# Performance work log

Hardware: AMD Instinct MI355X
Metric: run time of the kernel (lower is better)

The kernel has to match this reference:

```python
import jax, jax.numpy as jnp
import numpy as np

NUM_HEADS = 1


def setup_inputs() -> dict:
    key = jax.random.key(0)
    k1, k2, k3 = jax.random.split(key, 3)
    B, C, H, W = 32, 1024, 32, 32
    x = jax.random.normal(k1, (B, C, H, W), dtype=jnp.float32)
    w_qkv = jax.random.normal(k2, (3 * C, C), dtype=jnp.float32) * (C ** -0.5)
    w_proj = jax.random.normal(k3, (C, C), dtype=jnp.float32) * (C ** -0.5)
    b_proj = jnp.zeros((C,), dtype=jnp.float32)
    return {"x": x, "w_qkv": w_qkv, "w_proj": w_proj, "b_proj": b_proj}


def reference(x, w_qkv, w_proj, b_proj):
    B, C, H, W = x.shape
    nh = NUM_HEADS
    hd = C // nh
    S = H * W
    # 1x1 conv (no bias) == channel matmul
    qkv = jnp.einsum('bchw,oc->bohw', x, w_qkv)          # [B, 3C, H, W]
    qkv = qkv.reshape(B * nh, 3 * hd, S)
    q, k, v = jnp.split(qkv, 3, axis=1)                   # each [B*nh, hd, S]
    scale = hd ** -0.25
    attn = jax.nn.softmax(
        jnp.einsum('bct,bcs->bts', q * scale, k * scale), axis=-1)  # [B*nh, S, S]
    # faithful to source einsum 'bts,bcs->bts': sums v over channel dim only
    h = attn * jnp.sum(v, axis=1, keepdims=True)          # [B*nh, S, S]
    h = h.reshape(B, nh * S, H, W)                        # requires nh*S == C
    out = jnp.einsum('bchw,oc->bohw', h, w_proj) + b_proj[None, :, None, None]
    return out + x
```

## Files before the change

kernel.cpp:

```cpp
#include <hip/hip_runtime.h>
#include <hip/hip_bf16.h>
#include <stdint.h>


typedef __attribute__((ext_vector_type(8))) short short8;
typedef __attribute__((ext_vector_type(4))) short short4_t;
typedef __attribute__((ext_vector_type(4))) float f32x4;

__device__ __forceinline__ short f2b(float f) {
    __hip_bfloat16 h = __float2bfloat16(f);
    return *reinterpret_cast<short*>(&h);
}
__device__ __forceinline__ float b2f(short s) {
    __hip_bfloat16 h;
    *reinterpret_cast<short*>(&h) = s;
    return __bfloat162float(h);
}

#define GLOAD16(gp, lp) __builtin_amdgcn_global_load_lds(                      \
    (const __attribute__((address_space(1))) unsigned int*)(gp),               \
    (__attribute__((address_space(3))) unsigned int*)(lp), 16, 0, 0)

#define WAITV4 asm volatile("s_waitcnt vmcnt(4)" ::: "memory")
#define WAITV0 asm volatile("s_waitcnt vmcnt(0)" ::: "memory")
#define WAITL0 asm volatile("s_waitcnt lgkmcnt(0)" ::: "memory")
#define BAR()  { asm volatile("" ::: "memory"); __builtin_amdgcn_s_barrier(); \
                 asm volatile("" ::: "memory"); }

__global__ void k_wvsum(const float* __restrict__ wqkv, float* __restrict__ wvsum) {
    int c = blockIdx.x * 256 + threadIdx.x;
    int o0 = blockIdx.y * 32;
    float s = 0.f;
    const float* p = wqkv + (size_t)(2048 + o0) * 1024 + c;
    #pragma unroll 8
    for (int o = 0; o < 32; ++o) s += p[(size_t)o * 1024];
    atomicAdd(&wvsum[c], s);
}

__global__ void k_cvt(const float* __restrict__ in, short* __restrict__ out) {
    int i = (blockIdx.x * 256 + threadIdx.x) * 4;
    #pragma unroll
    for (int j = 0; j < 4; ++j) out[i + j] = f2b(in[i + j]);
}

__global__ void k_xpose(const float* __restrict__ x, const float* __restrict__ wvsum,
                        short* __restrict__ xT, float* __restrict__ vsum) {
    __shared__ float tile[32][33];
    __shared__ float ps[8][32];
    int b = blockIdx.z;
    int s0 = blockIdx.x * 32, c0 = blockIdx.y * 32;
    int tx = threadIdx.x, ty = threadIdx.y;
    const float* xb = x + ((size_t)b << 20);
    float p = 0.f;
    #pragma unroll
    for (int i = 0; i < 4; ++i) {
        int cl = ty + i * 8;
        float v = xb[(size_t)(c0 + cl) * 1024 + s0 + tx];
        tile[cl][tx] = v;
        p += v * wvsum[c0 + cl];
    }
    ps[ty][tx] = p;
    __syncthreads();
    short* xTb = xT + ((size_t)b << 20);
    #pragma unroll
    for (int i = 0; i < 4; ++i) {
        int sl = ty + i * 8;
        xTb[(size_t)(s0 + sl) * 1024 + c0 + tx] = f2b(tile[tx][sl]);
    }
    if (ty == 0) {
        float s = 0.f;
        #pragma unroll
        for (int i = 0; i < 8; ++i) s += ps[i][tx];
        atomicAdd(&vsum[b * 1024 + s0 + tx], s);
    }
}

__global__ void k_xposew(const float* __restrict__ wqkv, short* __restrict__ WT) {
    __shared__ float tile[32][33];
    int w = blockIdx.z;
    int o0 = blockIdx.x * 32, c0 = blockIdx.y * 32;
    int tx = threadIdx.x, ty = threadIdx.y;
    const float* src = wqkv + (size_t)w * 1048576;
    #pragma unroll
    for (int i = 0; i < 4; ++i)
        tile[ty + i * 8][tx] = src[(size_t)(o0 + ty + i * 8) * 1024 + c0 + tx];
    __syncthreads();
    short* dst = WT + (size_t)w * 1048576;
    #pragma unroll
    for (int i = 0; i < 4; ++i) {
        int cl = ty + i * 8;
        dst[(size_t)(c0 + cl) * 1024 + o0 + tx] = f2b(tile[tx][cl]);
    }
}

__global__ void k_red8(const float* __restrict__ part, short* __restrict__ MT) {
    int i4 = (blockIdx.x * 256 + threadIdx.x) * 4;
    f32x4 s = *(const f32x4*)&part[i4];
    #pragma unroll
    for (int z = 1; z < 8; ++z) s += *(const f32x4*)&part[(size_t)z * 1048576 + i4];
    short4_t r;
    #pragma unroll
    for (int j = 0; j < 4; ++j) r[j] = f2b(s[j]);
    *(short4_t*)&MT[i4] = r;
}

template <int MODE, int TM, int TN, int NT>
__global__ __launch_bounds__(512, 2)
void k_gemm(const short* __restrict__ A0, size_t strideA, int lda,
            const short* __restrict__ B0, size_t strideB, int ldb,
            void* __restrict__ O0, size_t strideO, int ldo,
            float* __restrict__ Z,
            const float* __restrict__ scale,
            const float* __restrict__ bias,
            const float* __restrict__ xres) {
    __shared__ __align__(16) short As[2 * 256 * 64];
    __shared__ __align__(16) short Bs[2 * 256 * 64];

    constexpr int TPB = TM * TN;
    int wg = blockIdx.x;
    int cpx = gridDim.x >> 3;
    int swz = (wg & 7) * cpx + (wg >> 3);
    int z = swz / TPB;
    int rz = swz - z * TPB;
    int m0 = (rz / TN) * 256, n0 = (rz % TN) * 256;

    int tid = threadIdx.x;
    int wid = tid >> 6, l = tid & 63;
    int wm = wid >> 2, wn = wid & 3;
    int lr = l & 15, lg = l >> 4;

    const short* A = A0 + (size_t)z * strideA;
    const short* Bt = B0 + (size_t)z * strideB;

    int srow = wid * 16 + (l >> 3);
    int scol = ((l & 7) ^ (l >> 3)) * 8;
    const short* gA = A + (size_t)(m0 + srow) * lda + scol;
    const short* gB = Bt + (size_t)(n0 + srow) * ldb + scol;
    char* const ldsA = (char*)As;
    char* const ldsB = (char*)Bs;
    int sdst = wid * 2048;

    auto SA = [&](int buf, int h, int t) __attribute__((always_inline)) {
        const short* g = gA + (size_t)(h * 128) * lda + t * 64;
        char* d = ldsA + buf * 32768 + h * 16384 + sdst;
        GLOAD16(g, d);
        GLOAD16(g + (size_t)8 * lda, d + 1024);
    };
    auto SB = [&](int buf, int h, int t) __attribute__((always_inline)) {
        const short* g = gB + (size_t)(h * 128) * ldb + t * 64;
        char* d = ldsB + buf * 32768 + h * 16384 + sdst;
        GLOAD16(g, d);
        GLOAD16(g + (size_t)8 * ldb, d + 1024);
    };

    int cs0 = ((lg) ^ (lr & 7)) * 16;
    int cs1 = ((4 + lg) ^ (lr & 7)) * 16;
    int arow = (wm * 128 + lr) * 128;
    int brow = (wn * 64 + lr) * 128;

    short8 af[8], bf0[4], bf1[4];
    f32x4 acc[8][4] = {};

    auto RDA = [&](int buf, int mh) __attribute__((always_inline)) {
        const char* p = ldsA + buf * 32768 + arow + mh * 8192;
        #pragma unroll
        for (int mi = 0; mi < 4; ++mi) {
            af[mi * 2]     = *(const short8*)(p + mi * 2048 + cs0);
            af[mi * 2 + 1] = *(const short8*)(p + mi * 2048 + cs1);
        }
    };
    auto RDB = [&](short8* dst, int buf, int nh) __attribute__((always_inline)) {
        const char* p = ldsB + buf * 32768 + brow + nh * 4096;
        #pragma unroll
        for (int ni = 0; ni < 2; ++ni) {
            dst[ni * 2]     = *(const short8*)(p + ni * 2048 + cs0);
            dst[ni * 2 + 1] = *(const short8*)(p + ni * 2048 + cs1);
        }
    };
    auto MMA = [&](const short8* bfp, int mh, int nh) __attribute__((always_inline)) {
        __builtin_amdgcn_s_setprio(1);
        #pragma unroll
        for (int ks = 0; ks < 2; ++ks)
            #pragma unroll
            for (int mi = 0; mi < 4; ++mi)
                #pragma unroll
                for (int ni = 0; ni < 2; ++ni)
                    acc[mh * 4 + mi][nh * 2 + ni] =
                        __builtin_amdgcn_mfma_f32_16x16x32_bf16(
                            af[mi * 2 + ks], bfp[ni * 2 + ks],
                            acc[mh * 4 + mi][nh * 2 + ni], 0, 0, 0);
        __builtin_amdgcn_s_setprio(0);
    };

    SB(0, 0, 0); SB(0, 1, 0); SA(0, 0, 0); SA(0, 1, 0);
    if constexpr (NT > 1) {
        SB(1, 0, 1); SB(1, 1, 1);
        WAITV4;
    } else {
        WAITV0;
    }
    BAR();

    #pragma unroll 2
    for (int t = 0; t < NT - 2; ++t) {
        int b = t & 1;
        RDA(b, 0); RDB(bf0, b, 0); SA(b ^ 1, 0, t + 1);
        BAR(); WAITL0; MMA(bf0, 0, 0); BAR();
        RDB(bf1, b, 1); SA(b ^ 1, 1, t + 1);
        BAR(); WAITL0; MMA(bf1, 0, 1); BAR();
        RDA(b, 1); SB(b, 0, t + 2);
        BAR(); WAITL0; MMA(bf0, 1, 0); BAR();
        SB(b, 1, t + 2); WAITV4;
        BAR(); MMA(bf1, 1, 1); BAR();
    }
    if constexpr (NT > 1) {
        constexpr int tp = NT - 2;
        constexpr int b = tp & 1;
        RDA(b, 0); RDB(bf0, b, 0); SA(b ^ 1, 0, NT - 1);
        BAR(); WAITL0; MMA(bf0, 0, 0); BAR();
        RDB(bf1, b, 1); SA(b ^ 1, 1, NT - 1);
        BAR(); WAITL0; MMA(bf1, 0, 1); BAR();
        RDA(b, 1);
        BAR(); WAITL0; MMA(bf0, 1, 0); BAR();
        WAITV0;
        BAR(); MMA(bf1, 1, 1); BAR();
    }
    {
        constexpr int b = (NT - 1) & 1;
        RDA(b, 0); RDB(bf0, b, 0);
        BAR(); WAITL0; MMA(bf0, 0, 0); BAR();
        RDB(bf1, b, 1);
        BAR(); WAITL0; MMA(bf1, 0, 1); BAR();
        RDA(b, 1);
        BAR(); WAITL0; MMA(bf0, 1, 0); BAR();
        MMA(bf1, 1, 1);
    }

    int rb = m0 + wm * 128, cb = n0 + wn * 64;
    if (MODE == 0) {
        short* O = (short*)O0 + (size_t)z * strideO;
        #pragma unroll
        for (int mi = 0; mi < 8; ++mi)
            #pragma unroll
            for (int ni = 0; ni < 4; ++ni)
                #pragma unroll
                for (int r = 0; r < 4; ++r)
                    O[(size_t)(rb + mi * 16 + lg * 4 + r) * ldo + cb + ni * 16 + lr] =
                        f2b(acc[mi][ni][r]);
    } else if (MODE == 1) {
        short* O = (short*)O0 + (size_t)z * strideO;
        float* Zb = Z + z * 1024;
        #pragma unroll
        for (int ni = 0; ni < 4; ++ni) {
            float zs = 0.f;
            #pragma unroll
            for (int mi = 0; mi < 8; ++mi)
                #pragma unroll
                for (int r = 0; r < 4; ++r) {
                    float ev = __expf(acc[mi][ni][r] * 0.03125f);
                    O[(size_t)(rb + mi * 16 + lg * 4 + r) * ldo + cb + ni * 16 + lr] = f2b(ev);
                    zs += ev;
                }
            zs += __shfl_xor(zs, 16);
            zs += __shfl_xor(zs, 32);
            if (l < 16) atomicAdd(&Zb[cb + ni * 16 + l], zs);
        }
    } else if (MODE == 2) {
        float* O = (float*)O0 + (size_t)z * strideO;
        const float* xr = xres + (size_t)z * strideO;
        #pragma unroll
        for (int mi = 0; mi < 8; ++mi)
            #pragma unroll
            for (int ni = 0; ni < 4; ++ni)
                #pragma unroll
                for (int r = 0; r < 4; ++r) {
                    int row = rb + mi * 16 + lg * 4 + r;
                    int col = cb + ni * 16 + lr;
                    O[(size_t)row * ldo + col] = acc[mi][ni][r] * scale[z * 1024 + col] +
                                                 bias[row] + xr[(size_t)row * ldo + col];
                }
    } else {
        float* O = (float*)O0 + (size_t)z * strideO;
        #pragma unroll
        for (int mi = 0; mi < 8; ++mi)
            #pragma unroll
            for (int ni = 0; ni < 4; ++ni)
                #pragma unroll
                for (int r = 0; r < 4; ++r)
                    O[(size_t)(rb + mi * 16 + lg * 4 + r) * ldo + cb + ni * 16 + lr] =
                        acc[mi][ni][r];
    }
}

__global__ void k_invz(float* Z) {
    int i = blockIdx.x * 256 + threadIdx.x;
    Z[i] = 1.0f / Z[i];
}

__global__ void k_wpscale(const short* __restrict__ wp_b, const float* __restrict__ invZ,
                          short* __restrict__ wp_s) {
    size_t i8 = ((size_t)blockIdx.x * 256 + threadIdx.x) * 8;
    int b = (int)(i8 >> 20);
    int t0 = (int)(i8 & 1023);
    short8 w = *(const short8*)&wp_b[i8 & 1048575];
    const float* iz = invZ + b * 1024 + t0;
    short8 r;
    #pragma unroll
    for (int j = 0; j < 8; ++j) r[j] = f2b(b2f(w[j]) * iz[j]);
    *(short8*)&wp_s[i8] = r;
}

extern "C" void kernel_launch(void* const* d_in, const int* in_sizes, int n_in,
                              void* d_out, int out_size, void* d_ws, size_t ws_size,
                              hipStream_t stream) {
    const float* x     = (const float*)d_in[0];
    const float* wqkv  = (const float*)d_in[1];
    const float* wproj = (const float*)d_in[2];
    const float* bproj = (const float*)d_in[3];
    float* out = (float*)d_out;

    char* ws = (char*)d_ws;
    size_t off = 0;
    auto alloc = [&](size_t bytes) {
        void* p = ws + off;
        off += (bytes + 255) & ~(size_t)255;
        return p;
    };
    float* wvsum = (float*)alloc(1024 * 4);
    short* wp_b  = (short*)alloc((size_t)1024 * 1024 * 2);
    short* xT    = (short*)alloc((size_t)32 * 1024 * 1024 * 2);
    short* WT    = (short*)alloc((size_t)2 * 1024 * 1024 * 2);
    float* MTp   = (float*)alloc((size_t)8 * 1024 * 1024 * 4);
    short* MT    = (short*)alloc((size_t)1024 * 1024 * 2);
    short* YT    = (short*)alloc((size_t)32 * 1024 * 1024 * 2);
    short* attnT = (short*)alloc((size_t)32 * 1024 * 1024 * 2);
    float* vsum  = (float*)alloc(32 * 1024 * 4);
    float* Zbuf  = (float*)alloc(32 * 1024 * 4);

    hipMemsetAsync(wvsum, 0, 1024 * 4, stream);
    hipMemsetAsync(vsum, 0, 32 * 1024 * 4, stream);
    hipMemsetAsync(Zbuf, 0, 32 * 1024 * 4, stream);

    k_wvsum<<<dim3(4, 32), 256, 0, stream>>>(wqkv, wvsum);
    k_cvt<<<1024, 256, 0, stream>>>(wproj, wp_b);
    k_xposew<<<dim3(32, 32, 2), dim3(32, 8), 0, stream>>>(wqkv, WT);
    k_xpose<<<dim3(32, 32, 32), dim3(32, 8), 0, stream>>>(x, wvsum, xT, vsum);

    k_gemm<3, 4, 4, 2><<<128, 512, 0, stream>>>(
        WT + 1048576, (size_t)128, 1024, WT, (size_t)128, 1024,
        MTp, (size_t)1048576, 1024, nullptr, nullptr, nullptr, nullptr);
    k_red8<<<1024, 256, 0, stream>>>(MTp, MT);

    k_gemm<0, 4, 4, 16><<<512, 512, 0, stream>>>(
        xT, (size_t)1048576, 1024, MT, 0, 1024,
        YT, (size_t)1048576, 1024, nullptr, nullptr, nullptr, nullptr);

    k_gemm<1, 4, 4, 16><<<512, 512, 0, stream>>>(
        xT, (size_t)1048576, 1024, YT, (size_t)1048576, 1024,
        attnT, (size_t)1048576, 1024, Zbuf, nullptr, nullptr, nullptr);

    k_invz<<<128, 256, 0, stream>>>(Zbuf);

    short* wp_s = xT;
    k_wpscale<<<16384, 256, 0, stream>>>(wp_b, Zbuf, wp_s);

    k_gemm<2, 4, 4, 16><<<512, 512, 0, stream>>>(
        wp_s, (size_t)1048576, 1024, attnT, (size_t)1048576, 1024,
        out, (size_t)1048576, 1024, nullptr, vsum, bproj, x);
}
```

Measured before the change: 362.7 us.

## Use smaller-tile 128x128 GEMM kernel for exp-score stage and fold reciprocal into scaling

Adds a new 256-thread GEMM kernel that uses 128x128 output tiles with a simple double-buffered K loop, and uses it for the exp/softmax-denominator stage with 2048 workgroups instead of 512 larger ones. The separate reciprocal kernel is removed, and the weight-scaling kernel divides by Z directly. This is meant to improve occupancy and load balance and drop one launch. In exchange the tiles are smaller, so there is less data reuse per tile, the pipeline is simpler, and there are more atomic adds into Z.

```diff
diff --git a/kernel.cpp b/kernel.cpp
--- a/kernel.cpp
+++ b/kernel.cpp
@@ -214,8 +214,7 @@
         BAR(); MMA(bf1, 1, 1); BAR();
     }
     if constexpr (NT > 1) {
-        constexpr int tp = NT - 2;
-        constexpr int b = tp & 1;
+        constexpr int b = (NT - 2) & 1;
         RDA(b, 0); RDB(bf0, b, 0); SA(b ^ 1, 0, NT - 1);
         BAR(); WAITL0; MMA(bf0, 0, 0); BAR();
         RDB(bf1, b, 1); SA(b ^ 1, 1, NT - 1);
@@ -292,21 +291,159 @@
     }
 }
 
-__global__ void k_invz(float* Z) {
-    int i = blockIdx.x * 256 + threadIdx.x;
-    Z[i] = 1.0f / Z[i];
-}
-
-__global__ void k_wpscale(const short* __restrict__ wp_b, const float* __restrict__ invZ,
+template <int MODE, int TM, int TN, int NT>
+__global__ __launch_bounds__(256)
+void k_g97(const short* __restrict__ A0, size_t strideA, int lda,
+           const short* __restrict__ B0, size_t strideB, int ldb,
+           void* __restrict__ O0, size_t strideO, int ldo,
+           float* __restrict__ Z,
+           const float* __restrict__ scale,
+           const float* __restrict__ bias,
+           const float* __restrict__ xres) {
+    __shared__ __align__(16) short As[2 * 128 * 32];
+    __shared__ __align__(16) short Bs[2 * 128 * 32];
+
+    constexpr int TPB = TM * TN;
+    int wg = blockIdx.x;
+    int cpx = gridDim.x >> 3;
+    int swz = (wg & 7) * cpx + (wg >> 3);
+    int z = swz / TPB;
+    int rz = swz - z * TPB;
+    int m0 = (rz / TN) * 128, n0 = (rz % TN) * 128;
+
+    int tid = threadIdx.x;
+    int wid = tid >> 6, l = tid & 63;
+    int wm = wid >> 1, wn = wid & 1;
+    int lr = l & 15, lg = l >> 4;
+
+    const short* A = A0 + (size_t)z * strideA;
+    const short* Bt = B0 + (size_t)z * strideB;
+
+    int srow = tid >> 2;
+    int schunk = (tid & 3) ^ ((tid >> 3) & 3);
+    const short* gA = A + (size_t)(m0 + srow) * lda + schunk * 8;
+    const short* gB = Bt + (size_t)(n0 + srow) * ldb + schunk * 8;
+    char* const ldsA = (char*)As;
+    char* const ldsB = (char*)Bs;
+    int sdst = tid * 16;
+
+    auto SA = [&](int buf, int t) __attribute__((always_inline)) {
+        GLOAD16(gA + t * 32,                      ldsA + buf * 8192 + sdst);
+        GLOAD16(gA + (size_t)64 * lda + t * 32,   ldsA + buf * 8192 + 4096 + sdst);
+    };
+    auto SB = [&](int buf, int t) __attribute__((always_inline)) {
+        GLOAD16(gB + t * 32,                      ldsB + buf * 8192 + sdst);
+        GLOAD16(gB + (size_t)64 * ldb + t * 32,   ldsB + buf * 8192 + 4096 + sdst);
+    };
+
+    int cs = (lg ^ ((lr >> 1) & 3)) * 16;
+    int arow = (wm * 64 + lr) * 64;
+    int brow = (wn * 64 + lr) * 64;
+
+    short8 af[4], bf[4];
+    f32x4 acc[4][4] = {};
+
+    auto RD = [&](int buf) __attribute__((always_inline)) {
+        const char* pa = ldsA + buf * 8192 + arow + cs;
+        const char* pb = ldsB + buf * 8192 + brow + cs;
+        #pragma unroll
+        for (int mi = 0; mi < 4; ++mi) af[mi] = *(const short8*)(pa + mi * 1024);
+        #pragma unroll
+        for (int ni = 0; ni < 4; ++ni) bf[ni] = *(const short8*)(pb + ni * 1024);
+    };
+    auto MMA = [&]() __attribute__((always_inline)) {
+        __builtin_amdgcn_s_setprio(1);
+        #pragma unroll
+        for (int mi = 0; mi < 4; ++mi)
+            #pragma unroll
+            for (int ni = 0; ni < 4; ++ni)
+                acc[mi][ni] = __builtin_amdgcn_mfma_f32_16x16x32_bf16(
+                    af[mi], bf[ni], acc[mi][ni], 0, 0, 0);
+        __builtin_amdgcn_s_setprio(0);
+    };
+
+    SA(0, 0); SB(0, 0);
+    WAITV0; BAR();
+
+    for (int t = 0; t < NT - 1; ++t) {
+        int b = t & 1;
+        SA(b ^ 1, t + 1); SB(b ^ 1, t + 1);
+        RD(b);
+        WAITL0; MMA();
+        WAITV0; BAR();
+    }
+    {
+        constexpr int b = (NT - 1) & 1;
+        RD(b);
+        WAITL0; MMA();
+    }
+
+    int rb = m0 + wm * 64, cb = n0 + wn * 64;
+    if (MODE == 0) {
+        short* O = (short*)O0 + (size_t)z * strideO;
+        #pragma unroll
+        for (int mi = 0; mi < 4; ++mi)
+            #pragma unroll
+            for (int ni = 0; ni < 4; ++ni)
+                #pragma unroll
+                for (int r = 0; r < 4; ++r)
+                    O[(size_t)(rb + mi * 16 + lg * 4 + r) * ldo + cb + ni * 16 + lr] =
+                        f2b(acc[mi][ni][r]);
+    } else if (MODE == 1) {
+        short* O = (short*)O0 + (size_t)z * strideO;
+        float* Zb = Z + z * 1024;
+        #pragma unroll
+        for (int ni = 0; ni < 4; ++ni) {
+            float zs = 0.f;
+            #pragma unroll
+            for (int mi = 0; mi < 4; ++mi)
+                #pragma unroll
+                for (int r = 0; r < 4; ++r) {
+                    float ev = __expf(acc[mi][ni][r] * 0.03125f);
+                    O[(size_t)(rb + mi * 16 + lg * 4 + r) * ldo + cb + ni * 16 + lr] = f2b(ev);
+                    zs += ev;
+                }
+            zs += __shfl_xor(zs, 16);
+            zs += __shfl_xor(zs, 32);
+            if (l < 16) atomicAdd(&Zb[cb + ni * 16 + l], zs);
+        }
+    } else if (MODE == 2) {
+        float* O = (float*)O0 + (size_t)z * strideO;
+        const float* xr = xres + (size_t)z * strideO;
+        #pragma unroll
+        for (int mi = 0; mi < 4; ++mi)
+            #pragma unroll
+            for (int ni = 0; ni < 4; ++ni)
+                #pragma unroll
+                for (int r = 0; r < 4; ++r) {
+                    int row = rb + mi * 16 + lg * 4 + r;
+                    int col = cb + ni * 16 + lr;
+                    O[(size_t)row * ldo + col] = acc[mi][ni][r] * scale[z * 1024 + col] +
+                                                 bias[row] + xr[(size_t)row * ldo + col];
+                }
+    } else {
+        float* O = (float*)O0 + (size_t)z * strideO;
+        #pragma unroll
+        for (int mi = 0; mi < 4; ++mi)
+            #pragma unroll
+            for (int ni = 0; ni < 4; ++ni)
+                #pragma unroll
+                for (int r = 0; r < 4; ++r)
+                    O[(size_t)(rb + mi * 16 + lg * 4 + r) * ldo + cb + ni * 16 + lr] =
+                        acc[mi][ni][r];
+    }
+}
+
+__global__ void k_wpscale(const short* __restrict__ wp_b, const float* __restrict__ Zr,
                           short* __restrict__ wp_s) {
     size_t i8 = ((size_t)blockIdx.x * 256 + threadIdx.x) * 8;
     int b = (int)(i8 >> 20);
     int t0 = (int)(i8 & 1023);
     short8 w = *(const short8*)&wp_b[i8 & 1048575];
-    const float* iz = invZ + b * 1024 + t0;
+    const float* zp = Zr + b * 1024 + t0;
     short8 r;
     #pragma unroll
-    for (int j = 0; j < 8; ++j) r[j] = f2b(b2f(w[j]) * iz[j]);
+    for (int j = 0; j < 8; ++j) r[j] = f2b(b2f(w[j]) / zp[j]);
     *(short8*)&wp_s[i8] = r;
 }
 
@@ -355,11 +492,9 @@
         xT, (size_t)1048576, 1024, MT, 0, 1024,
         YT, (size_t)1048576, 1024, nullptr, nullptr, nullptr, nullptr);
 
-    k_gemm<1, 4, 4, 16><<<512, 512, 0, stream>>>(
+    k_g97<1, 8, 8, 32><<<2048, 256, 0, stream>>>(
         xT, (size_t)1048576, 1024, YT, (size_t)1048576, 1024,
         attnT, (size_t)1048576, 1024, Zbuf, nullptr, nullptr, nullptr);
-
-    k_invz<<<128, 256, 0, stream>>>(Zbuf);
 
     short* wp_s = xT;
     k_wpscale<<<16384, 256, 0, stream>>>(wp_b, Zbuf, wp_s);
```

Result: slower. 377.6 us (+4.1%).

## Process two N-tiles per workgroup with continuous pipelined K-loop across segments

Applied to the files above, without the earlier changes.

Adds a k_gseg kernel in which each workgroup computes two 256x256 output tiles sharing the same A rows (column offsets n00 and n00+512). The software pipeline keeps running across the tile boundary, so loads for the second tile start during the tail of the first. The three big batched GEMMs now launch 256 workgroups instead of 512. The separate reciprocal kernel is removed and its work folded into k_wpscale as a divide. The intent is to cut the pipeline prologue/epilogue cost and launch overhead, at the risk of lower parallelism with half as many workgroups and longer-lived accumulators.

```diff
diff --git a/kernel.cpp b/kernel.cpp
--- a/kernel.cpp
+++ b/kernel.cpp
@@ -214,8 +214,7 @@
         BAR(); MMA(bf1, 1, 1); BAR();
     }
     if constexpr (NT > 1) {
-        constexpr int tp = NT - 2;
-        constexpr int b = tp & 1;
+        constexpr int b = (NT - 2) & 1;
         RDA(b, 0); RDB(bf0, b, 0); SA(b ^ 1, 0, NT - 1);
         BAR(); WAITL0; MMA(bf0, 0, 0); BAR();
         RDB(bf1, b, 1); SA(b ^ 1, 1, NT - 1);
@@ -237,7 +236,17 @@
     }
 
     int rb = m0 + wm * 128, cb = n0 + wn * 64;
-    if (MODE == 0) {
+    if (MODE == 3) {
+        float* O = (float*)O0 + (size_t)z * strideO;
+        #pragma unroll
+        for (int mi = 0; mi < 8; ++mi)
+            #pragma unroll
+            for (int ni = 0; ni < 4; ++ni)
+                #pragma unroll
+                for (int r = 0; r < 4; ++r)
+                    O[(size_t)(rb + mi * 16 + lg * 4 + r) * ldo + cb + ni * 16 + lr] =
+                        acc[mi][ni][r];
+    } else {
         short* O = (short*)O0 + (size_t)z * strideO;
         #pragma unroll
         for (int mi = 0; mi < 8; ++mi)
@@ -247,66 +256,211 @@
                 for (int r = 0; r < 4; ++r)
                     O[(size_t)(rb + mi * 16 + lg * 4 + r) * ldo + cb + ni * 16 + lr] =
                         f2b(acc[mi][ni][r]);
-    } else if (MODE == 1) {
-        short* O = (short*)O0 + (size_t)z * strideO;
-        float* Zb = Z + z * 1024;
-        #pragma unroll
-        for (int ni = 0; ni < 4; ++ni) {
-            float zs = 0.f;
+    }
+}
+
+template <int MODE, int NT>
+__global__ __launch_bounds__(512, 2)
+void k_gseg(const short* __restrict__ A0, size_t strideA, int lda,
+            const short* __restrict__ B0, size_t strideB, int ldb,
+            void* __restrict__ O0, size_t strideO, int ldo,
+            float* __restrict__ Z,
+            const float* __restrict__ scale,
+            const float* __restrict__ bias,
+            const float* __restrict__ xres) {
+    __shared__ __align__(16) short As[2 * 256 * 64];
+    __shared__ __align__(16) short Bs[2 * 256 * 64];
+
+    int wg = blockIdx.x;
+    int cpx = gridDim.x >> 3;
+    int swz = (wg & 7) * cpx + (wg >> 3);
+    int z = swz >> 3;
+    int rz = swz & 7;
+    int m0 = (rz >> 1) * 256;
+    int n00 = (rz & 1) * 256;
+
+    int tid = threadIdx.x;
+    int wid = tid >> 6, l = tid & 63;
+    int wm = wid >> 2, wn = wid & 3;
+    int lr = l & 15, lg = l >> 4;
+
+    const short* A = A0 + (size_t)z * strideA;
+    const short* Bt = B0 + (size_t)z * strideB;
+
+    int srow = wid * 16 + (l >> 3);
+    int scol = ((l & 7) ^ (l >> 3)) * 8;
+    const short* gA = A + (size_t)(m0 + srow) * lda + scol;
+    const short* gB0 = Bt + (size_t)(n00 + srow) * ldb + scol;
+    const short* gB1 = gB0 + (size_t)512 * ldb;
+    char* const ldsA = (char*)As;
+    char* const ldsB = (char*)Bs;
+    int sdst = wid * 2048;
+
+    auto SA = [&](int buf, int h, int k) __attribute__((always_inline)) {
+        const short* g = gA + (size_t)(h * 128) * lda + k * 64;
+        char* d = ldsA + buf * 32768 + h * 16384 + sdst;
+        GLOAD16(g, d);
+        GLOAD16(g + (size_t)8 * lda, d + 1024);
+    };
+    auto SBp = [&](const short* gBb, int buf, int h, int k) __attribute__((always_inline)) {
+        const short* g = gBb + (size_t)(h * 128) * ldb + k * 64;
+        char* d = ldsB + buf * 32768 + h * 16384 + sdst;
+        GLOAD16(g, d);
+        GLOAD16(g + (size_t)8 * ldb, d + 1024);
+    };
+
+    int cs0 = ((lg) ^ (lr & 7)) * 16;
+    int cs1 = ((4 + lg) ^ (lr & 7)) * 16;
+    int arow = (wm * 128 + lr) * 128;
+    int brow = (wn * 64 + lr) * 128;
+
+    short8 af[8], bf0[4], bf1[4];
+    f32x4 acc[8][4] = {};
+
+    auto RDA = [&](int buf, int mh) __attribute__((always_inline)) {
+        const char* p = ldsA + buf * 32768 + arow + mh * 8192;
+        #pragma unroll
+        for (int mi = 0; mi < 4; ++mi) {
+            af[mi * 2]     = *(const short8*)(p + mi * 2048 + cs0);
+            af[mi * 2 + 1] = *(const short8*)(p + mi * 2048 + cs1);
+        }
+    };
+    auto RDB = [&](short8* dst, int buf, int nh) __attribute__((always_inline)) {
+        const char* p = ldsB + buf * 32768 + brow + nh * 4096;
+        #pragma unroll
+        for (int ni = 0; ni < 2; ++ni) {
+            dst[ni * 2]     = *(const short8*)(p + ni * 2048 + cs0);
+            dst[ni * 2 + 1] = *(const short8*)(p + ni * 2048 + cs1);
+        }
+    };
+    auto MMA = [&](const short8* bfp, int mh, int nh) __attribute__((always_inline)) {
+        __builtin_amdgcn_s_setprio(1);
+        #pragma unroll
+        for (int ks = 0; ks < 2; ++ks)
+            #pragma unroll
+            for (int mi = 0; mi < 4; ++mi)
+                #pragma unroll
+                for (int ni = 0; ni < 2; ++ni)
+                    acc[mh * 4 + mi][nh * 2 + ni] =
+                        __builtin_amdgcn_mfma_f32_16x16x32_bf16(
+                            af[mi * 2 + ks], bfp[ni * 2 + ks],
+                            acc[mh * 4 + mi][nh * 2 + ni], 0, 0, 0);
+        __builtin_amdgcn_s_setprio(0);
+    };
+
+    auto BODY = [&](int b, int kA, int kB, const short* gBs) __attribute__((always_inline)) {
+        RDA(b, 0); RDB(bf0, b, 0); SA(b ^ 1, 0, kA);
+        BAR(); WAITL0; MMA(bf0, 0, 0); BAR();
+        RDB(bf1, b, 1); SA(b ^ 1, 1, kA);
+        BAR(); WAITL0; MMA(bf1, 0, 1); BAR();
+        RDA(b, 1); SBp(gBs, b, 0, kB);
+        BAR(); WAITL0; MMA(bf0, 1, 0); BAR();
+        SBp(gBs, b, 1, kB); WAITV4;
+        BAR(); MMA(bf1, 1, 1); BAR();
+    };
+
+    auto STORE = [&](int nbase) __attribute__((always_inline)) {
+        int rb = m0 + wm * 128, cb = nbase + wn * 64;
+        if (MODE == 0) {
+            short* O = (short*)O0 + (size_t)z * strideO;
             #pragma unroll
             for (int mi = 0; mi < 8; ++mi)
                 #pragma unroll
-                for (int r = 0; r < 4; ++r) {
-                    float ev = __expf(acc[mi][ni][r] * 0.03125f);
-                    O[(size_t)(rb + mi * 16 + lg * 4 + r) * ldo + cb + ni * 16 + lr] = f2b(ev);
-                    zs += ev;
-                }
-            zs += __shfl_xor(zs, 16);
-            zs += __shfl_xor(zs, 32);
-            if (l < 16) atomicAdd(&Zb[cb + ni * 16 + l], zs);
+                for (int ni = 0; ni < 4; ++ni)
+                    #pragma unroll
+                    for (int r = 0; r < 4; ++r)
+                        O[(size_t)(rb + mi * 16 + lg * 4 + r) * ldo + cb + ni * 16 + lr] =
+                            f2b(acc[mi][ni][r]);
+        } else if (MODE == 1) {
+            short* O = (short*)O0 + (size_t)z * strideO;
+            float* Zb = Z + z * 1024;
+            #pragma unroll
+            for (int ni = 0; ni < 4; ++ni) {
+                float zs = 0.f;
+                #pragma unroll
+                for (int mi = 0; mi < 8; ++mi)
+                    #pragma unroll
+                    for (int r = 0; r < 4; ++r) {
+                        float ev = __expf(acc[mi][ni][r] * 0.03125f);
+                        O[(size_t)(rb + mi * 16 + lg * 4 + r) * ldo + cb + ni * 16 + lr] = f2b(ev);
+                        zs += ev;
+                    }
+                zs += __shfl_xor(zs, 16);
+                zs += __shfl_xor(zs, 32);
+                if (l < 16) atomicAdd(&Zb[cb + ni * 16 + l], zs);
+            }
+        } else {
+            float* O = (float*)O0 + (size_t)z * strideO;
+            const float* xr = xres + (size_t)z * strideO;
+            #pragma unroll
+            for (int mi = 0; mi < 8; ++mi)
+                #pragma unroll
+                for (int ni = 0; ni < 4; ++ni)
+                    #pragma unroll
+                    for (int r = 0; r < 4; ++r) {
+                        int row = rb + mi * 16 + lg * 4 + r;
+                        int col = cb + ni * 16 + lr;
+                        O[(size_t)row * ldo + col] = acc[mi][ni][r] * scale[z * 1024 + col] +
+                                                     bias[row] + xr[(size_t)row * ldo + col];
+                    }
         }
-    } else if (MODE == 2) {
-        float* O = (float*)O0 + (size_t)z * strideO;
-        const float* xr = xres + (size_t)z * strideO;
-        #pragma unroll
-        for (int mi = 0; mi < 8; ++mi)
-            #pragma unroll
-            for (int ni = 0; ni < 4; ++ni)
-                #pragma unroll
-                for (int r = 0; r < 4; ++r) {
-                    int row = rb + mi * 16 + lg * 4 + r;
-                    int col = cb + ni * 16 + lr;
-                    O[(size_t)row * ldo + col] = acc[mi][ni][r] * scale[z * 1024 + col] +
-                                                 bias[row] + xr[(size_t)row * ldo + col];
-                }
-    } else {
-        float* O = (float*)O0 + (size_t)z * strideO;
-        #pragma unroll
-        for (int mi = 0; mi < 8; ++mi)
-            #pragma unroll
-            for (int ni = 0; ni < 4; ++ni)
-                #pragma unroll
-                for (int r = 0; r < 4; ++r)
-                    O[(size_t)(rb + mi * 16 + lg * 4 + r) * ldo + cb + ni * 16 + lr] =
-                        acc[mi][ni][r];
-    }
-}
-
-__global__ void k_invz(float* Z) {
-    int i = blockIdx.x * 256 + threadIdx.x;
-    Z[i] = 1.0f / Z[i];
-}
-
-__global__ void k_wpscale(const short* __restrict__ wp_b, const float* __restrict__ invZ,
+    };
+
+    SBp(gB0, 0, 0, 0); SBp(gB0, 0, 1, 0); SA(0, 0, 0); SA(0, 1, 0);
+    SBp(gB0, 1, 0, 1); SBp(gB0, 1, 1, 1);
+    WAITV4;
+    BAR();
+
+    #pragma unroll 2
+    for (int t = 0; t < NT - 2; ++t)
+        BODY(t & 1, t + 1, t + 2, gB0);
+    BODY((NT - 2) & 1, NT - 1, 0, gB1);
+    BODY((NT - 1) & 1, 0, 1, gB1);
+
+    STORE(n00);
+    #pragma unroll
+    for (int mi = 0; mi < 8; ++mi)
+        #pragma unroll
+        for (int ni = 0; ni < 4; ++ni)
+            acc[mi][ni] = (f32x4){0.f, 0.f, 0.f, 0.f};
+
+    #pragma unroll 2
+    for (int t = NT; t < 2 * NT - 2; ++t)
+        BODY(t & 1, (t + 1) & (NT - 1), (t + 2) & (NT - 1), gB1);
+    {
+        constexpr int b = 0;
+        RDA(b, 0); RDB(bf0, b, 0); SA(b ^ 1, 0, NT - 1);
+        BAR(); WAITL0; MMA(bf0, 0, 0); BAR();
+        RDB(bf1, b, 1); SA(b ^ 1, 1, NT - 1);
+        BAR(); WAITL0; MMA(bf1, 0, 1); BAR();
+        RDA(b, 1);
+        BAR(); WAITL0; MMA(bf0, 1, 0); BAR();
+        WAITV0;
+        BAR(); MMA(bf1, 1, 1); BAR();
+    }
+    {
+        constexpr int b = 1;
+        RDA(b, 0); RDB(bf0, b, 0);
+        BAR(); WAITL0; MMA(bf0, 0, 0); BAR();
+        RDB(bf1, b, 1);
+        BAR(); WAITL0; MMA(bf1, 0, 1); BAR();
+        RDA(b, 1);
+        BAR(); WAITL0; MMA(bf0, 1, 0); BAR();
+        MMA(bf1, 1, 1);
+    }
+    STORE(n00 + 512);
+}
+
+__global__ void k_wpscale(const short* __restrict__ wp_b, const float* __restrict__ Zr,
                           short* __restrict__ wp_s) {
     size_t i8 = ((size_t)blockIdx.x * 256 + threadIdx.x) * 8;
     int b = (int)(i8 >> 20);
     int t0 = (int)(i8 & 1023);
     short8 w = *(const short8*)&wp_b[i8 & 1048575];
-    const float* iz = invZ + b * 1024 + t0;
+    const float* zp = Zr + b * 1024 + t0;
     short8 r;
     #pragma unroll
-    for (int j = 0; j < 8; ++j) r[j] = f2b(b2f(w[j]) * iz[j]);
+    for (int j = 0; j < 8; ++j) r[j] = f2b(b2f(w[j]) / zp[j]);
     *(short8*)&wp_s[i8] = r;
 }
 
@@ -351,20 +505,18 @@
         MTp, (size_t)1048576, 1024, nullptr, nullptr, nullptr, nullptr);
     k_red8<<<1024, 256, 0, stream>>>(MTp, MT);
 
-    k_gemm<0, 4, 4, 16><<<512, 512, 0, stream>>>(
+    k_gseg<0, 16><<<256, 512, 0, stream>>>(
         xT, (size_t)1048576, 1024, MT, 0, 1024,
         YT, (size_t)1048576, 1024, nullptr, nullptr, nullptr, nullptr);
 
-    k_gemm<1, 4, 4, 16><<<512, 512, 0, stream>>>(
+    k_gseg<1, 16><<<256, 512, 0, stream>>>(
         xT, (size_t)1048576, 1024, YT, (size_t)1048576, 1024,
         attnT, (size_t)1048576, 1024, Zbuf, nullptr, nullptr, nullptr);
 
-    k_invz<<<128, 256, 0, stream>>>(Zbuf);
-
     short* wp_s = xT;
     k_wpscale<<<16384, 256, 0, stream>>>(wp_b, Zbuf, wp_s);
 
-    k_gemm<2, 4, 4, 16><<<512, 512, 0, stream>>>(
+    k_gseg<2, 16><<<256, 512, 0, stream>>>(
         wp_s, (size_t)1048576, 1024, attnT, (size_t)1048576, 1024,
         out, (size_t)1048576, 1024, nullptr, vsum, bproj, x);
 }
```

Result: slower. 467.8 us (+29.0%).
